# Kernel optimization log

Hardware: AMD Instinct MI355X
Metric: run time of the kernel (lower is better)

## Reference

```python
import jax, jax.numpy as jnp
import numpy as np

N_NODES = 100000
N_EDGES = 3200000
D_IN = 64
D_Z = 64
D_OUT = 3
SQRT_D = 0.1
SIGMA = (0.01, 0.01, 0.01)


def _seg_softmax(scores, seg, n):
    # softmax over edges grouped by destination node (PyG `softmax`)
    m = jax.ops.segment_max(scores, seg, num_segments=n)
    e = jnp.exp(scores - m[seg])
    s = jax.ops.segment_sum(e, seg, num_segments=n)
    return e / (s[seg] + 1e-16)


def _tconv(x, src, dst, Wq, bq, Wk, bk, Wv, bv, Ws, bs):
    # PyG TransformerConv, heads=1, concat=True, root_weight=True, beta=False
    n = x.shape[0]
    c = Wq.shape[1]
    q = x @ Wq + bq                                   # [N, C]
    k = x @ Wk + bk
    v = x @ Wv + bv
    scores = jnp.sum(q[dst] * k[src], axis=-1) / jnp.sqrt(jnp.asarray(c, x.dtype))  # [E]
    alpha = _seg_softmax(scores, dst, n)              # [E]
    agg = jax.ops.segment_sum(v[src] * alpha[:, None], dst, num_segments=n)  # [N, C]
    return agg + x @ Ws + bs                          # skip connection (lin_skip)


def _lin_params(key, din, dout):
    kw, kb = jax.random.split(key)
    scale = 1.0 / np.sqrt(din)
    W = jax.random.uniform(kw, (din, dout), jnp.float32, -scale, scale)
    b = jax.random.uniform(kb, (dout,), jnp.float32, -scale, scale)
    return W, b


def setup_inputs() -> dict:
    key = jax.random.key(0)
    keys = jax.random.split(key, 16)
    x = jax.random.normal(keys[0], (N_NODES, D_IN), jnp.float32)
    edge_index = jax.random.randint(keys[1], (2, N_EDGES), 0, N_NODES, jnp.int32)
    noise = jax.random.normal(keys[2], (N_NODES, D_OUT), jnp.float32)
    inp = {"x": x, "edge_index": edge_index, "noise": noise}
    dims = [(D_IN, D_Z), (D_Z, D_Z), (D_Z, D_OUT)]
    ki = 3
    for li, (din, dout) in enumerate(dims, start=1):
        for nm in ("q", "k", "v", "s"):
            W, b = _lin_params(keys[ki], din, dout)
            ki += 1
            inp[f"W{li}{nm}"] = W
            inp[f"b{li}{nm}"] = b
    return inp


def reference(x, edge_index, noise,
              W1q, b1q, W1k, b1k, W1v, b1v, W1s, b1s,
              W2q, b2q, W2k, b2k, W2v, b2v, W2s, b2s,
              W3q, b3q, W3k, b3k, W3v, b3v, W3s, b3s):
    src, dst = edge_index[0], edge_index[1]
    h = jnp.tanh(_tconv(x, src, dst, W1q, b1q, W1k, b1k, W1v, b1v, W1s, b1s))
    h = jnp.tanh(_tconv(h, src, dst, W2q, b2q, W2k, b2k, W2v, b2v, W2s, b2s) + h)
    drift = _tconv(h, src, dst, W3q, b3q, W3k, b3k, W3v, b3v, W3s, b3s)  # [N, 3]
    sigma = jnp.asarray(SIGMA, drift.dtype)
    z = noise * sigma  # per-column noise scaling (std_z > 1e-4 branch)
    return drift + z / SQRT_D
```

## Files before the change

kernel.cpp:

```cpp
#include <hip/hip_runtime.h>

#define N_NODES 100000
#define N_EDGES 3200000
#define NBUK 391
#define NPB 256
#define CHUNK 8192
#define NCHUNK 391

#if defined(__has_builtin)
#if __has_builtin(__builtin_amdgcn_fdot2_f32_bf16)
#define HAS_DOT2 1
#endif
#endif
#ifndef HAS_DOT2
#define HAS_DOT2 0
#endif

__device__ __forceinline__ float bf2f(unsigned short u) {
  return __uint_as_float(((unsigned)u) << 16);
}
__device__ __forceinline__ unsigned short f2bf(float f) {
  unsigned u = __float_as_uint(f);
  u += 0x7fffu + ((u >> 16) & 1u);
  return (unsigned short)(u >> 16);
}
__device__ __forceinline__ float lo16(unsigned u) { return __uint_as_float(u << 16); }
__device__ __forceinline__ float hi16(unsigned u) { return __uint_as_float(u & 0xffff0000u); }


__global__ void k_detect(const unsigned short* __restrict__ xu, int* __restrict__ flag) {
  __shared__ int cnt;
  if (threadIdx.x == 0) cnt = 0;
  __syncthreads();
  int c = 0;
  for (int i = threadIdx.x; i < 4096; i += 256) {
    float v = fabsf(bf2f(xu[2 * i]));
    if (v >= 1e-4f && v <= 10.f) c++;
  }
  atomicAdd(&cnt, c);
  __syncthreads();
  if (threadIdx.x == 0) *flag = (cnt > 2048) ? 1 : 0;
}


__global__ __launch_bounds__(512) void k_cvt_x(const void* __restrict__ x,
                                               unsigned short* __restrict__ xb,
                                               const int* __restrict__ flag) {
  int i = blockIdx.x * 512 + threadIdx.x;
  if (i >= N_NODES * 8) return;
  if (*flag) {
    ((uint4*)xb)[i] = ((const uint4*)x)[i];
  } else {
    const float4* xf = (const float4*)x;
    float4 a = xf[2 * i], b = xf[2 * i + 1];
    uint4 o;
    o.x = (unsigned)f2bf(a.x) | ((unsigned)f2bf(a.y) << 16);
    o.y = (unsigned)f2bf(a.z) | ((unsigned)f2bf(a.w) << 16);
    o.z = (unsigned)f2bf(b.x) | ((unsigned)f2bf(b.y) << 16);
    o.w = (unsigned)f2bf(b.z) | ((unsigned)f2bf(b.w) << 16);
    ((uint4*)xb)[i] = o;
  }
}

struct CvtArgs {
  const void* src[24];
  int dstoff[24];
  int n[24];
  int pp[24];
};

__global__ void k_cvt_w(CvtArgs a, unsigned short* __restrict__ wb,
                        const int* __restrict__ flag) {
  int b = blockIdx.x;
  const void* s = a.src[b];
  int n = a.n[b];
  int pp = a.pp[b];
  unsigned short* d = wb + a.dstoff[b];
  int isbf = *flag;
  for (int i = threadIdx.x; i < n; i += 256) {
    unsigned short v = isbf ? ((const unsigned short*)s)[i] : f2bf(((const float*)s)[i]);
    if (pp) {
      int k = i >> 6, c = i & 63;
      d[((k >> 1) << 7) + (c << 1) + (k & 1)] = v;
    } else {
      d[i] = v;
    }
  }
}


__global__ __launch_bounds__(256) void k_bhist(const int* __restrict__ dsts,
                                               int* __restrict__ counts) {
  __shared__ int hist[NBUK];
  for (int i = threadIdx.x; i < NBUK; i += 256) hist[i] = 0;
  __syncthreads();
  int e0 = blockIdx.x * CHUNK;
  int n = min(CHUNK, N_EDGES - e0);
  for (int i = threadIdx.x; i < n; i += 256)
    atomicAdd(&hist[dsts[e0 + i] >> 8], 1);
  __syncthreads();
  for (int i = threadIdx.x; i < NBUK; i += 256)
    counts[blockIdx.x * NBUK + i] = hist[i];
}

__global__ __launch_bounds__(64) void k_bscanA(int* __restrict__ counts,
                                               int* __restrict__ tot) {
  int b = blockIdx.x;
  int lane = threadIdx.x;
  int carry = 0;
  for (int c0 = 0; c0 < NCHUNK; c0 += 64) {
    int c = c0 + lane;
    int v = (c < NCHUNK) ? counts[c * NBUK + b] : 0;
    int s = v;
#pragma unroll
    for (int o = 1; o < 64; o <<= 1) {
      int u = __shfl_up(s, o, 64);
      if (lane >= o) s += u;
    }
    if (c < NCHUNK) counts[c * NBUK + b] = s - v + carry;
    carry += __shfl(s, 63, 64);
  }
  if (lane == 0) tot[b] = carry;
}

__global__ void k_bscanB(const int* __restrict__ tot, int* __restrict__ bbase) {
  __shared__ int s[512];
  int t = threadIdx.x;
  int v = (t < NBUK) ? tot[t] : 0;
  s[t] = v;
  __syncthreads();
  for (int o = 1; o < 512; o <<= 1) {
    int u = (t >= o) ? s[t - o] : 0;
    __syncthreads();
    s[t] += u;
    __syncthreads();
  }
  if (t <= NBUK) bbase[t] = s[t] - v;
}

__global__ __launch_bounds__(256) void k_bscat(const int* __restrict__ srcs,
                                               const int* __restrict__ dsts,
                                               const int* __restrict__ counts,
                                               const int* __restrict__ bbase,
                                               unsigned* __restrict__ blist) {
  __shared__ int cnt[NBUK];
  for (int i = threadIdx.x; i < NBUK; i += 256)
    cnt[i] = counts[blockIdx.x * NBUK + i] + bbase[i];
  __syncthreads();
  int e0 = blockIdx.x * CHUNK;
  int n = min(CHUNK, N_EDGES - e0);
  for (int i = threadIdx.x; i < n; i += 256) {
    int s = srcs[e0 + i];
    int d = dsts[e0 + i];
    int p = atomicAdd(&cnt[d >> 8], 1);
    blist[p] = ((unsigned)s << 8) | (unsigned)(d & 255);
  }
}

__global__ __launch_bounds__(256) void k_bfinal(const unsigned* __restrict__ blist,
                                                const int* __restrict__ bbase,
                                                int* __restrict__ off,
                                                int* __restrict__ csr) {
  __shared__ int hcnt[NPB];
  __shared__ int sc[NPB];
  int t = threadIdx.x;
  int b = blockIdx.x;
  int s = bbase[b], e = bbase[b + 1];
  hcnt[t] = 0;
  __syncthreads();
  for (int i = s + t; i < e; i += 256)
    atomicAdd(&hcnt[blist[i] & 255], 1);
  __syncthreads();
  int v = hcnt[t];
  sc[t] = v;
  __syncthreads();
  for (int o = 1; o < 256; o <<= 1) {
    int u = (t >= o) ? sc[t - o] : 0;
    __syncthreads();
    sc[t] += u;
    __syncthreads();
  }
  int my = s + sc[t] - v;
  int node = b * NPB + t;
  if (node < N_NODES) off[node] = my;
  if (b == 0 && t == 0) off[N_NODES] = bbase[NBUK];
  sc[t] = my;
  __syncthreads();
  for (int i = s + t; i < e; i += 256) {
    unsigned u = blist[i];
    int p = atomicAdd(&sc[u & 255], 1);
    csr[p] = (int)(u >> 8);
  }
}


#if HAS_DOT2
typedef __bf16 bf16x2 __attribute__((ext_vector_type(2)));
__device__ __forceinline__ float dot2bf(unsigned h2, unsigned w2, float acc) {
  return __builtin_amdgcn_fdot2_f32_bf16(__builtin_bit_cast(bf16x2, h2),
                                         __builtin_bit_cast(bf16x2, w2), acc, false);
}
#else
__device__ __forceinline__ float dot2bf(unsigned h2, unsigned w2, float acc) {
  acc += lo16(h2) * lo16(w2);
  acc += hi16(h2) * hi16(w2);
  return acc;
}
#endif

__global__ __launch_bounds__(256) void k_gemmkvqs(
    const unsigned short* __restrict__ hin,
    const unsigned* __restrict__ PQ2, const unsigned* __restrict__ PK2,
    const unsigned* __restrict__ PV2, const unsigned* __restrict__ PS2,
    const unsigned short* __restrict__ bq, const unsigned short* __restrict__ bk,
    const unsigned short* __restrict__ bv, const unsigned short* __restrict__ bs,
    unsigned short* __restrict__ Kt, unsigned short* __restrict__ Vt,
    float* __restrict__ Qt, float* __restrict__ St) {
  int wid = blockIdx.x * 4 + (threadIdx.x >> 6);
  int lane = threadIdx.x & 63;
  int r0 = wid * 4;
  const unsigned* hrow = (const unsigned*)(hin + (size_t)r0 * 64);
  unsigned hp0 = hrow[lane & 31];
  unsigned hp1 = hrow[32 + (lane & 31)];
  unsigned hp2 = hrow[64 + (lane & 31)];
  unsigned hp3 = hrow[96 + (lane & 31)];
  float bqv = bf2f(bq[lane]), bkv = bf2f(bk[lane]);
  float bvv = bf2f(bv[lane]), bsv = bf2f(bs[lane]);
  float qa0 = bqv, qa1 = bqv, qa2 = bqv, qa3 = bqv;
  float ka0 = bkv, ka1 = bkv, ka2 = bkv, ka3 = bkv;
  float va0 = bvv, va1 = bvv, va2 = bvv, va3 = bvv;
  float sa0 = bsv, sa1 = bsv, sa2 = bsv, sa3 = bsv;
  for (int kk = 0; kk < 32; ++kk) {
    unsigned wq = PQ2[kk * 64 + lane];
    unsigned wk = PK2[kk * 64 + lane];
    unsigned wv = PV2[kk * 64 + lane];
    unsigned ws = PS2[kk * 64 + lane];
    unsigned hb0 = __shfl(hp0, kk, 64);
    unsigned hb1 = __shfl(hp1, kk, 64);
    unsigned hb2 = __shfl(hp2, kk, 64);
    unsigned hb3 = __shfl(hp3, kk, 64);
    qa0 = dot2bf(hb0, wq, qa0); ka0 = dot2bf(hb0, wk, ka0);
    va0 = dot2bf(hb0, wv, va0); sa0 = dot2bf(hb0, ws, sa0);
    qa1 = dot2bf(hb1, wq, qa1); ka1 = dot2bf(hb1, wk, ka1);
    va1 = dot2bf(hb1, wv, va1); sa1 = dot2bf(hb1, ws, sa1);
    qa2 = dot2bf(hb2, wq, qa2); ka2 = dot2bf(hb2, wk, ka2);
    va2 = dot2bf(hb2, wv, va2); sa2 = dot2bf(hb2, ws, sa2);
    qa3 = dot2bf(hb3, wq, qa3); ka3 = dot2bf(hb3, wk, ka3);
    va3 = dot2bf(hb3, wv, va3); sa3 = dot2bf(hb3, ws, sa3);
  }
  Kt[(size_t)(r0 + 0) * 64 + lane] = f2bf(ka0);
  Kt[(size_t)(r0 + 1) * 64 + lane] = f2bf(ka1);
  Kt[(size_t)(r0 + 2) * 64 + lane] = f2bf(ka2);
  Kt[(size_t)(r0 + 3) * 64 + lane] = f2bf(ka3);
  Vt[(size_t)(r0 + 0) * 64 + lane] = f2bf(va0);
  Vt[(size_t)(r0 + 1) * 64 + lane] = f2bf(va1);
  Vt[(size_t)(r0 + 2) * 64 + lane] = f2bf(va2);
  Vt[(size_t)(r0 + 3) * 64 + lane] = f2bf(va3);
  Qt[(size_t)(r0 + 0) * 64 + lane] = qa0;
  Qt[(size_t)(r0 + 1) * 64 + lane] = qa1;
  Qt[(size_t)(r0 + 2) * 64 + lane] = qa2;
  Qt[(size_t)(r0 + 3) * 64 + lane] = qa3;
  St[(size_t)(r0 + 0) * 64 + lane] = sa0;
  St[(size_t)(r0 + 1) * 64 + lane] = sa1;
  St[(size_t)(r0 + 2) * 64 + lane] = sa2;
  St[(size_t)(r0 + 3) * 64 + lane] = sa3;
}


template <bool RES>
__global__ __launch_bounds__(256) void k_edge64b(
    const int* __restrict__ off, const int* __restrict__ csr,
    const unsigned short* __restrict__ hin,
    const float* __restrict__ Qt, const float* __restrict__ St,
    const unsigned short* __restrict__ Kt, const unsigned short* __restrict__ Vt,
    unsigned short* __restrict__ hout) {
  __shared__ float qs[4][64];
  int w = threadIdx.x >> 6;
  int lane = threadIdx.x & 63;
  int wid = blockIdx.x * 4 + w;
  int base = off[wid];
  int deg = off[wid + 1] - base;
  int nsrc = csr[base + ((lane < deg) ? lane : 0)];
  float q = Qt[(size_t)wid * 64 + lane];
  float sk = St[(size_t)wid * 64 + lane];
  float hv = 0.f;
  if (RES) hv = bf2f(hin[(size_t)wid * 64 + lane]);
  qs[w][lane] = q;

  float m = -1e30f, ssum = 0.f;
  float4 acc = {0.f, 0.f, 0.f, 0.f};
  int g = lane >> 4;
  int c16 = lane & 15;
  int g8 = lane >> 3;
  int c8 = lane & 7;
  const float4* qv = (const float4*)qs[w];
  float4 qA = qv[2 * c8];
  float4 qB = qv[2 * c8 + 1];

  for (int j0 = 0; j0 < deg; j0 += 64) {
    int cnt = min(64, deg - j0);
    int src = nsrc;
    int nj = j0 + 64;
    if (nj < deg)
      nsrc = csr[base + nj + ((lane < deg - nj) ? lane : 0)];
    float sc = 0.f;
    int nit = (cnt + 7) >> 3;
    for (int t = 0; t < nit; ++t) {
      int st = __shfl(src, 8 * t + g8, 64);
      uint4 kk = *(const uint4*)(Kt + (size_t)st * 64 + c8 * 8);
      float p = qA.x * lo16(kk.x) + qA.y * hi16(kk.x)
              + qA.z * lo16(kk.y) + qA.w * hi16(kk.y)
              + qB.x * lo16(kk.z) + qB.y * hi16(kk.z)
              + qB.z * lo16(kk.w) + qB.w * hi16(kk.w);
      p += __shfl_xor(p, 4, 64);
      p += __shfl_xor(p, 2, 64);
      p += __shfl_xor(p, 1, 64);
      float got = __shfl(p, (lane & 7) << 3, 64);
      if ((lane >> 3) == t) sc = got;
    }
    sc *= 0.125f;
    sc = fminf(fmaxf(sc, -60.f), 60.f);
    if (lane >= cnt) sc = -1e30f;
    float bm = sc;
    bm = fmaxf(bm, __shfl_xor(bm, 32, 64));
    bm = fmaxf(bm, __shfl_xor(bm, 16, 64));
    bm = fmaxf(bm, __shfl_xor(bm, 8, 64));
    bm = fmaxf(bm, __shfl_xor(bm, 4, 64));
    bm = fmaxf(bm, __shfl_xor(bm, 2, 64));
    bm = fmaxf(bm, __shfl_xor(bm, 1, 64));
    float mn = fmaxf(m, bm);
    float al = __expf(sc - mn);
    float bsum = al;
    bsum += __shfl_xor(bsum, 32, 64);
    bsum += __shfl_xor(bsum, 16, 64);
    bsum += __shfl_xor(bsum, 8, 64);
    bsum += __shfl_xor(bsum, 4, 64);
    bsum += __shfl_xor(bsum, 2, 64);
    bsum += __shfl_xor(bsum, 1, 64);
    float corr = __expf(m - mn);
    ssum = ssum * corr + bsum;
    acc.x *= corr;
    acc.y *= corr;
    acc.z *= corr;
    acc.w *= corr;
    m = mn;
    for (int jj = 0; jj < cnt; jj += 16) {
      int e0 = jj + g, e1 = jj + 4 + g, e2 = jj + 8 + g, e3 = jj + 12 + g;
      int s0 = __shfl(src, e0, 64);
      int s1 = __shfl(src, e1, 64);
      int s2 = __shfl(src, e2, 64);
      int s3 = __shfl(src, e3, 64);
      float a0 = __shfl(al, e0, 64);
      float a1 = __shfl(al, e1, 64);
      float a2 = __shfl(al, e2, 64);
      float a3 = __shfl(al, e3, 64);
      uint2 v0 = *(const uint2*)(Vt + (size_t)s0 * 64 + c16 * 4);
      uint2 v1 = *(const uint2*)(Vt + (size_t)s1 * 64 + c16 * 4);
      uint2 v2 = *(const uint2*)(Vt + (size_t)s2 * 64 + c16 * 4);
      uint2 v3 = *(const uint2*)(Vt + (size_t)s3 * 64 + c16 * 4);
      acc.x += a0 * lo16(v0.x); acc.y += a0 * hi16(v0.x);
      acc.z += a0 * lo16(v0.y); acc.w += a0 * hi16(v0.y);
      acc.x += a1 * lo16(v1.x); acc.y += a1 * hi16(v1.x);
      acc.z += a1 * lo16(v1.y); acc.w += a1 * hi16(v1.y);
      acc.x += a2 * lo16(v2.x); acc.y += a2 * hi16(v2.x);
      acc.z += a2 * lo16(v2.y); acc.w += a2 * hi16(v2.y);
      acc.x += a3 * lo16(v3.x); acc.y += a3 * hi16(v3.x);
      acc.z += a3 * lo16(v3.y); acc.w += a3 * hi16(v3.y);
    }
  }
  acc.x += __shfl_xor(acc.x, 16, 64);
  acc.y += __shfl_xor(acc.y, 16, 64);
  acc.z += __shfl_xor(acc.z, 16, 64);
  acc.w += __shfl_xor(acc.w, 16, 64);
  acc.x += __shfl_xor(acc.x, 32, 64);
  acc.y += __shfl_xor(acc.y, 32, 64);
  acc.z += __shfl_xor(acc.z, 32, 64);
  acc.w += __shfl_xor(acc.w, 32, 64);
  float f0 = __shfl(acc.x, lane >> 2, 64);
  float f1 = __shfl(acc.y, lane >> 2, 64);
  float f2 = __shfl(acc.z, lane >> 2, 64);
  float f3 = __shfl(acc.w, lane >> 2, 64);
  int cc = lane & 3;
  float aggv = (cc == 0) ? f0 : ((cc == 1) ? f1 : ((cc == 2) ? f2 : f3));
  float val = aggv / (ssum + 1e-16f) + sk;
  if (RES) val += hv;
  hout[(size_t)wid * 64 + lane] = f2bf(tanhf(val));
}


__global__ __launch_bounds__(256) void k_gemm3(
    const unsigned short* __restrict__ hin,
    const unsigned short* __restrict__ Wq, const unsigned short* __restrict__ bq,
    const unsigned short* __restrict__ Wk, const unsigned short* __restrict__ bk,
    const unsigned short* __restrict__ Wv, const unsigned short* __restrict__ bv,
    const unsigned short* __restrict__ Ws, const unsigned short* __restrict__ bs,
    float* __restrict__ Q3, float* __restrict__ S3, uint4* __restrict__ KV3) {
  int r = blockIdx.x * 4 + (threadIdx.x >> 6);
  int lane = threadIdx.x & 63;
  float hj = bf2f(hin[(size_t)r * 64 + lane]);
  float p[12];
#pragma unroll
  for (int c = 0; c < 3; ++c) {
    p[c]     = hj * bf2f(Wq[lane * 3 + c]);
    p[3 + c] = hj * bf2f(Wk[lane * 3 + c]);
    p[6 + c] = hj * bf2f(Wv[lane * 3 + c]);
    p[9 + c] = hj * bf2f(Ws[lane * 3 + c]);
  }
#pragma unroll
  for (int o = 32; o >= 1; o >>= 1) {
#pragma unroll
    for (int i = 0; i < 12; ++i) p[i] += __shfl_xor(p[i], o, 64);
  }
  if (lane == 0) {
    float kk[3], vv[3];
    for (int c = 0; c < 3; ++c) {
      Q3[r * 4 + c] = p[c] + bf2f(bq[c]);
      S3[r * 4 + c] = p[9 + c] + bf2f(bs[c]);
      kk[c] = p[3 + c] + bf2f(bk[c]);
      vv[c] = p[6 + c] + bf2f(bv[c]);
    }
    uint4 pk;
    pk.x = (unsigned)f2bf(kk[0]) | ((unsigned)f2bf(vv[0]) << 16);
    pk.y = (unsigned)f2bf(kk[1]) | ((unsigned)f2bf(vv[1]) << 16);
    pk.z = (unsigned)f2bf(kk[2]) | ((unsigned)f2bf(vv[2]) << 16);
    pk.w = 0;
    KV3[r] = pk;
  }
}


__global__ __launch_bounds__(256) void k_edge3(
    const int* __restrict__ off, const int* __restrict__ csr,
    const float* __restrict__ Q3, const float* __restrict__ S3,
    const uint4* __restrict__ KV3, const void* __restrict__ noise,
    void* __restrict__ out, const int* __restrict__ flag) {
  int w = threadIdx.x >> 6;
  int lane = threadIdx.x & 63;
  int d = blockIdx.x * 4 + w;
  int base = off[d];
  int deg = off[d + 1] - base;
  float q0 = Q3[d * 4], q1 = Q3[d * 4 + 1], q2 = Q3[d * 4 + 2];
  const float isq = 0.57735026919f;
  float m = -1e30f, ssum = 0.f, a0 = 0.f, a1 = 0.f, a2 = 0.f;
  for (int j0 = 0; j0 < deg; j0 += 64) {
    int cnt = min(64, deg - j0);
    int src = csr[base + ((lane < cnt) ? (j0 + lane) : 0)];
    uint4 kv = KV3[src];
    float sc = (q0 * lo16(kv.x) + q1 * lo16(kv.y) + q2 * lo16(kv.z)) * isq;
    sc = fminf(fmaxf(sc, -60.f), 60.f);
    if (lane >= cnt) sc = -1e30f;
    float bm = sc;
#pragma unroll
    for (int o = 32; o >= 1; o >>= 1) bm = fmaxf(bm, __shfl_xor(bm, o, 64));
    float mn = fmaxf(m, bm);
    float al = __expf(sc - mn);
    float p0 = al * hi16(kv.x);
    float p1 = al * hi16(kv.y);
    float p2 = al * hi16(kv.z);
    float bsum = al;
#pragma unroll
    for (int o = 32; o >= 1; o >>= 1) {
      bsum += __shfl_xor(bsum, o, 64);
      p0 += __shfl_xor(p0, o, 64);
      p1 += __shfl_xor(p1, o, 64);
      p2 += __shfl_xor(p2, o, 64);
    }
    float corr = __expf(m - mn);
    ssum = ssum * corr + bsum;
    a0 = a0 * corr + p0;
    a1 = a1 * corr + p1;
    a2 = a2 * corr + p2;
    m = mn;
  }
  if (lane == 0) {
    float inv = 1.f / (ssum + 1e-16f);
    int isbf = *flag;
    float n0, n1, n2;
    if (isbf) {
      const unsigned short* nu = (const unsigned short*)noise;
      n0 = bf2f(nu[d * 3 + 0]);
      n1 = bf2f(nu[d * 3 + 1]);
      n2 = bf2f(nu[d * 3 + 2]);
    } else {
      const float* nf = (const float*)noise;
      n0 = nf[d * 3 + 0];
      n1 = nf[d * 3 + 1];
      n2 = nf[d * 3 + 2];
    }
    float r0 = a0 * inv + S3[d * 4 + 0] + 0.1f * n0;
    float r1 = a1 * inv + S3[d * 4 + 1] + 0.1f * n1;
    float r2 = a2 * inv + S3[d * 4 + 2] + 0.1f * n2;
    if (isbf) {
      unsigned short* ou = (unsigned short*)out;
      ou[d * 3 + 0] = f2bf(r0);
      ou[d * 3 + 1] = f2bf(r1);
      ou[d * 3 + 2] = f2bf(r2);
    } else {
      float* of = (float*)out;
      of[d * 3 + 0] = r0;
      of[d * 3 + 1] = r1;
      of[d * 3 + 2] = r2;
    }
  }
}


extern "C" void kernel_launch(void* const* d_in, const int* in_sizes, int n_in,
                              void* d_out, int out_size, void* d_ws, size_t ws_size,
                              hipStream_t stream) {
  const int* ei = (const int*)d_in[1];
  const int* srcs = ei;
  const int* dsts = ei + N_EDGES;

  char* w = (char*)d_ws;
  int* off = (int*)w;
  int* csr = (int*)(w + 400128);
  char* hreg = w + 13200128;
  unsigned short* h = (unsigned short*)hreg;
  int* counts = (int*)(hreg + 524288);
  int* bbase = (int*)(hreg + 1200128);
  int* tot = (int*)(hreg + 1310720);
  char* kvbase = w + 26000128;
  unsigned* blist = (unsigned*)kvbase;
  unsigned short* Kt = (unsigned short*)kvbase;
  unsigned short* Vt = (unsigned short*)(kvbase + 12800000);
  float* Q3 = (float*)kvbase;
  float* S3 = (float*)(kvbase + 2097152);
  uint4* KV3 = (uint4*)(kvbase + 4194304);
  unsigned short* wb = (unsigned short*)(w + 51600128);
  int* flag = (int*)(w + 51668352);
  float* Qt = (float*)(w + 51668480);
  float* St = (float*)(w + 77268480);
  const size_t NEED_BIG = 102868480;
  if (ws_size < NEED_BIG) return;

  CvtArgs ca;
  {
    int idx = 0;
    for (int l = 0; l < 2; ++l) {
      int base = l * 16640;
      for (int p = 0; p < 4; ++p) {
        ca.src[idx] = d_in[3 + l * 8 + p * 2];
        ca.dstoff[idx] = base + p * 4096;
        ca.n[idx] = 4096;
        ca.pp[idx] = 1;
        idx++;
        ca.src[idx] = d_in[3 + l * 8 + p * 2 + 1];
        ca.dstoff[idx] = base + 16384 + p * 64;
        ca.n[idx] = 64;
        ca.pp[idx] = 0;
        idx++;
      }
    }
    int o = 33280;
    for (int p = 0; p < 4; ++p) {
      ca.src[idx] = d_in[3 + 16 + p * 2];
      ca.dstoff[idx] = o;
      ca.n[idx] = 192;
      ca.pp[idx] = 0;
      o += 192;
      idx++;
      ca.src[idx] = d_in[3 + 16 + p * 2 + 1];
      ca.dstoff[idx] = o;
      ca.n[idx] = 3;
      ca.pp[idx] = 0;
      o += 3;
      idx++;
    }
  }
  const unsigned* PQ20 = (const unsigned*)(wb);
  const unsigned* PK20 = (const unsigned*)(wb + 4096);
  const unsigned* PV20 = (const unsigned*)(wb + 8192);
  const unsigned* PS20 = (const unsigned*)(wb + 12288);
  const unsigned* PQ21 = (const unsigned*)(wb + 16640);
  const unsigned* PK21 = (const unsigned*)(wb + 16640 + 4096);
  const unsigned* PV21 = (const unsigned*)(wb + 16640 + 8192);
  const unsigned* PS21 = (const unsigned*)(wb + 16640 + 12288);
  const unsigned short* Bq0 = wb + 16384;
  const unsigned short* Bk0 = wb + 16448;
  const unsigned short* Bv0 = wb + 16512;
  const unsigned short* Bs0 = wb + 16576;
  const unsigned short* Bq1 = wb + 16640 + 16384;
  const unsigned short* Bk1 = wb + 16640 + 16448;
  const unsigned short* Bv1 = wb + 16640 + 16512;
  const unsigned short* Bs1 = wb + 16640 + 16576;
  const unsigned short* W3q = wb + 33280;
  const unsigned short* B3q = wb + 33472;
  const unsigned short* W3k = wb + 33475;
  const unsigned short* B3k = wb + 33667;
  const unsigned short* W3v = wb + 33670;
  const unsigned short* B3v = wb + 33862;
  const unsigned short* W3s = wb + 33865;
  const unsigned short* B3s = wb + 34057;

  k_detect<<<1, 256, 0, stream>>>((const unsigned short*)d_in[0], flag);
  k_cvt_w<<<24, 256, 0, stream>>>(ca, wb, flag);

  k_bhist<<<NCHUNK, 256, 0, stream>>>(dsts, counts);
  k_bscanA<<<NBUK, 64, 0, stream>>>(counts, tot);
  k_bscanB<<<1, 512, 0, stream>>>(tot, bbase);
  k_bscat<<<NCHUNK, 256, 0, stream>>>(srcs, dsts, counts, bbase, blist);
  k_bfinal<<<NBUK, 256, 0, stream>>>(blist, bbase, off, csr);

  k_cvt_x<<<(N_NODES * 8 + 511) / 512, 512, 0, stream>>>(d_in[0], h, flag);

  const int gw = N_NODES / 4;
  const int gp = N_NODES / 16;
  k_gemmkvqs<<<gp, 256, 0, stream>>>(h, PQ20, PK20, PV20, PS20,
                                     Bq0, Bk0, Bv0, Bs0, Kt, Vt, Qt, St);
  k_edge64b<false><<<gw, 256, 0, stream>>>(off, csr, h, Qt, St, Kt, Vt, h);
  k_gemmkvqs<<<gp, 256, 0, stream>>>(h, PQ21, PK21, PV21, PS21,
                                     Bq1, Bk1, Bv1, Bs1, Kt, Vt, Qt, St);
  k_edge64b<true><<<gw, 256, 0, stream>>>(off, csr, h, Qt, St, Kt, Vt, h);
  k_gemm3<<<gw, 256, 0, stream>>>(h, W3q, B3q, W3k, B3k, W3v, B3v, W3s, B3s,
                                  Q3, S3, KV3);
  k_edge3<<<gw, 256, 0, stream>>>(off, csr, Q3, S3, KV3, d_in[2], d_out, flag);
}
```

Measured before the change: 649.4 us.

## Fuse x conversion into first GEMM, widen GEMM rows, repack layer-3 weights

Removes the separate x-to-bf16 conversion kernel by converting fp32 input rows inside the first projection GEMM. The GEMM now handles 8 rows per wave instead of 4, so each weight load serves more rows. The layer-3 projection is rewritten to pack its weights as bf16 pairs and spread each node's dot products over 4 lanes with dot2, replacing the full 64-lane reductions. The edge kernel also broadcasts q with shuffles instead of staging it through shared memory. The costs are more register pressure in the GEMM and extra shuffles in the edge kernel.

```diff
diff --git a/kernel.cpp b/kernel.cpp
--- a/kernel.cpp
+++ b/kernel.cpp
@@ -40,26 +40,6 @@
   atomicAdd(&cnt, c);
   __syncthreads();
   if (threadIdx.x == 0) *flag = (cnt > 2048) ? 1 : 0;
-}
-
-
-__global__ __launch_bounds__(512) void k_cvt_x(const void* __restrict__ x,
-                                               unsigned short* __restrict__ xb,
-                                               const int* __restrict__ flag) {
-  int i = blockIdx.x * 512 + threadIdx.x;
-  if (i >= N_NODES * 8) return;
-  if (*flag) {
-    ((uint4*)xb)[i] = ((const uint4*)x)[i];
-  } else {
-    const float4* xf = (const float4*)x;
-    float4 a = xf[2 * i], b = xf[2 * i + 1];
-    uint4 o;
-    o.x = (unsigned)f2bf(a.x) | ((unsigned)f2bf(a.y) << 16);
-    o.y = (unsigned)f2bf(a.z) | ((unsigned)f2bf(a.w) << 16);
-    o.z = (unsigned)f2bf(b.x) | ((unsigned)f2bf(b.y) << 16);
-    o.w = (unsigned)f2bf(b.z) | ((unsigned)f2bf(b.w) << 16);
-    ((uint4*)xb)[i] = o;
-  }
 }
 
 struct CvtArgs {
@@ -79,9 +59,12 @@
   int isbf = *flag;
   for (int i = threadIdx.x; i < n; i += 256) {
     unsigned short v = isbf ? ((const unsigned short*)s)[i] : f2bf(((const float*)s)[i]);
-    if (pp) {
+    if (pp == 1) {
       int k = i >> 6, c = i & 63;
       d[((k >> 1) << 7) + (c << 1) + (k & 1)] = v;
+    } else if (pp >= 3) {
+      int dd = i / 3, c = i % 3 + (pp - 3);
+      d[(dd >> 1) * 24 + (c << 1) + (dd & 1)] = v;
     } else {
       d[i] = v;
     }
@@ -208,8 +191,9 @@
 }
 #endif
 
+template <bool L1>
 __global__ __launch_bounds__(256) void k_gemmkvqs(
-    const unsigned short* __restrict__ hin,
+    const void* __restrict__ xin, const int* __restrict__ flag,
     const unsigned* __restrict__ PQ2, const unsigned* __restrict__ PK2,
     const unsigned* __restrict__ PV2, const unsigned* __restrict__ PS2,
     const unsigned short* __restrict__ bq, const unsigned short* __restrict__ bk,
@@ -218,52 +202,54 @@
     float* __restrict__ Qt, float* __restrict__ St) {
   int wid = blockIdx.x * 4 + (threadIdx.x >> 6);
   int lane = threadIdx.x & 63;
-  int r0 = wid * 4;
-  const unsigned* hrow = (const unsigned*)(hin + (size_t)r0 * 64);
-  unsigned hp0 = hrow[lane & 31];
-  unsigned hp1 = hrow[32 + (lane & 31)];
-  unsigned hp2 = hrow[64 + (lane & 31)];
-  unsigned hp3 = hrow[96 + (lane & 31)];
+  int r0 = wid * 8;
+  int l31 = lane & 31;
+  unsigned hp[8];
+  bool cvt = L1 && (*flag == 0);
+  if (cvt) {
+    const float2* xf = (const float2*)xin;
+#pragma unroll
+    for (int j = 0; j < 8; ++j) {
+      float2 v = xf[(size_t)(r0 + j) * 32 + l31];
+      hp[j] = (unsigned)f2bf(v.x) | ((unsigned)f2bf(v.y) << 16);
+    }
+  } else {
+    const unsigned* hu = (const unsigned*)xin;
+#pragma unroll
+    for (int j = 0; j < 8; ++j)
+      hp[j] = hu[(size_t)(r0 + j) * 32 + l31];
+  }
   float bqv = bf2f(bq[lane]), bkv = bf2f(bk[lane]);
   float bvv = bf2f(bv[lane]), bsv = bf2f(bs[lane]);
-  float qa0 = bqv, qa1 = bqv, qa2 = bqv, qa3 = bqv;
-  float ka0 = bkv, ka1 = bkv, ka2 = bkv, ka3 = bkv;
-  float va0 = bvv, va1 = bvv, va2 = bvv, va3 = bvv;
-  float sa0 = bsv, sa1 = bsv, sa2 = bsv, sa3 = bsv;
+  float qa[8], ka[8], va[8], sa[8];
+#pragma unroll
+  for (int j = 0; j < 8; ++j) {
+    qa[j] = bqv;
+    ka[j] = bkv;
+    va[j] = bvv;
+    sa[j] = bsv;
+  }
   for (int kk = 0; kk < 32; ++kk) {
     unsigned wq = PQ2[kk * 64 + lane];
     unsigned wk = PK2[kk * 64 + lane];
     unsigned wv = PV2[kk * 64 + lane];
     unsigned ws = PS2[kk * 64 + lane];
-    unsigned hb0 = __shfl(hp0, kk, 64);
-    unsigned hb1 = __shfl(hp1, kk, 64);
-    unsigned hb2 = __shfl(hp2, kk, 64);
-    unsigned hb3 = __shfl(hp3, kk, 64);
-    qa0 = dot2bf(hb0, wq, qa0); ka0 = dot2bf(hb0, wk, ka0);
-    va0 = dot2bf(hb0, wv, va0); sa0 = dot2bf(hb0, ws, sa0);
-    qa1 = dot2bf(hb1, wq, qa1); ka1 = dot2bf(hb1, wk, ka1);
-    va1 = dot2bf(hb1, wv, va1); sa1 = dot2bf(hb1, ws, sa1);
-    qa2 = dot2bf(hb2, wq, qa2); ka2 = dot2bf(hb2, wk, ka2);
-    va2 = dot2bf(hb2, wv, va2); sa2 = dot2bf(hb2, ws, sa2);
-    qa3 = dot2bf(hb3, wq, qa3); ka3 = dot2bf(hb3, wk, ka3);
-    va3 = dot2bf(hb3, wv, va3); sa3 = dot2bf(hb3, ws, sa3);
-  }
-  Kt[(size_t)(r0 + 0) * 64 + lane] = f2bf(ka0);
-  Kt[(size_t)(r0 + 1) * 64 + lane] = f2bf(ka1);
-  Kt[(size_t)(r0 + 2) * 64 + lane] = f2bf(ka2);
-  Kt[(size_t)(r0 + 3) * 64 + lane] = f2bf(ka3);
-  Vt[(size_t)(r0 + 0) * 64 + lane] = f2bf(va0);
-  Vt[(size_t)(r0 + 1) * 64 + lane] = f2bf(va1);
-  Vt[(size_t)(r0 + 2) * 64 + lane] = f2bf(va2);
-  Vt[(size_t)(r0 + 3) * 64 + lane] = f2bf(va3);
-  Qt[(size_t)(r0 + 0) * 64 + lane] = qa0;
-  Qt[(size_t)(r0 + 1) * 64 + lane] = qa1;
-  Qt[(size_t)(r0 + 2) * 64 + lane] = qa2;
-  Qt[(size_t)(r0 + 3) * 64 + lane] = qa3;
-  St[(size_t)(r0 + 0) * 64 + lane] = sa0;
-  St[(size_t)(r0 + 1) * 64 + lane] = sa1;
-  St[(size_t)(r0 + 2) * 64 + lane] = sa2;
-  St[(size_t)(r0 + 3) * 64 + lane] = sa3;
+#pragma unroll
+    for (int j = 0; j < 8; ++j) {
+      unsigned hb = __shfl(hp[j], kk, 64);
+      qa[j] = dot2bf(hb, wq, qa[j]);
+      ka[j] = dot2bf(hb, wk, ka[j]);
+      va[j] = dot2bf(hb, wv, va[j]);
+      sa[j] = dot2bf(hb, ws, sa[j]);
+    }
+  }
+#pragma unroll
+  for (int j = 0; j < 8; ++j) {
+    Kt[(size_t)(r0 + j) * 64 + lane] = f2bf(ka[j]);
+    Vt[(size_t)(r0 + j) * 64 + lane] = f2bf(va[j]);
+    Qt[(size_t)(r0 + j) * 64 + lane] = qa[j];
+    St[(size_t)(r0 + j) * 64 + lane] = sa[j];
+  }
 }
 
 
@@ -274,7 +260,6 @@
     const float* __restrict__ Qt, const float* __restrict__ St,
     const unsigned short* __restrict__ Kt, const unsigned short* __restrict__ Vt,
     unsigned short* __restrict__ hout) {
-  __shared__ float qs[4][64];
   int w = threadIdx.x >> 6;
   int lane = threadIdx.x & 63;
   int wid = blockIdx.x * 4 + w;
@@ -285,7 +270,6 @@
   float sk = St[(size_t)wid * 64 + lane];
   float hv = 0.f;
   if (RES) hv = bf2f(hin[(size_t)wid * 64 + lane]);
-  qs[w][lane] = q;
 
   float m = -1e30f, ssum = 0.f;
   float4 acc = {0.f, 0.f, 0.f, 0.f};
@@ -293,9 +277,16 @@
   int c16 = lane & 15;
   int g8 = lane >> 3;
   int c8 = lane & 7;
-  const float4* qv = (const float4*)qs[w];
-  float4 qA = qv[2 * c8];
-  float4 qB = qv[2 * c8 + 1];
+  int b8 = c8 << 3;
+  float4 qA, qB;
+  qA.x = __shfl(q, b8 + 0, 64);
+  qA.y = __shfl(q, b8 + 1, 64);
+  qA.z = __shfl(q, b8 + 2, 64);
+  qA.w = __shfl(q, b8 + 3, 64);
+  qB.x = __shfl(q, b8 + 4, 64);
+  qB.y = __shfl(q, b8 + 5, 64);
+  qB.z = __shfl(q, b8 + 6, 64);
+  qB.w = __shfl(q, b8 + 7, 64);
 
   for (int j0 = 0; j0 < deg; j0 += 64) {
     int cnt = min(64, deg - j0);
@@ -389,42 +380,52 @@
 
 
 __global__ __launch_bounds__(256) void k_gemm3(
-    const unsigned short* __restrict__ hin,
-    const unsigned short* __restrict__ Wq, const unsigned short* __restrict__ bq,
-    const unsigned short* __restrict__ Wk, const unsigned short* __restrict__ bk,
-    const unsigned short* __restrict__ Wv, const unsigned short* __restrict__ bv,
-    const unsigned short* __restrict__ Ws, const unsigned short* __restrict__ bs,
+    const unsigned short* __restrict__ hin, const unsigned* __restrict__ W12p,
+    const unsigned short* __restrict__ bq, const unsigned short* __restrict__ bk,
+    const unsigned short* __restrict__ bv, const unsigned short* __restrict__ bs,
     float* __restrict__ Q3, float* __restrict__ S3, uint4* __restrict__ KV3) {
-  int r = blockIdx.x * 4 + (threadIdx.x >> 6);
+  int w = threadIdx.x >> 6;
   int lane = threadIdx.x & 63;
-  float hj = bf2f(hin[(size_t)r * 64 + lane]);
-  float p[12];
-#pragma unroll
-  for (int c = 0; c < 3; ++c) {
-    p[c]     = hj * bf2f(Wq[lane * 3 + c]);
-    p[3 + c] = hj * bf2f(Wk[lane * 3 + c]);
-    p[6 + c] = hj * bf2f(Wv[lane * 3 + c]);
-    p[9 + c] = hj * bf2f(Ws[lane * 3 + c]);
-  }
-#pragma unroll
-  for (int o = 32; o >= 1; o >>= 1) {
-#pragma unroll
-    for (int i = 0; i < 12; ++i) p[i] += __shfl_xor(p[i], o, 64);
-  }
-  if (lane == 0) {
+  int g = lane >> 2, q4 = lane & 3;
+  int node = blockIdx.x * 64 + w * 16 + g;
+  if (node >= N_NODES) return;
+  const uint4* hp = (const uint4*)(hin + (size_t)node * 64 + q4 * 16);
+  uint4 h0 = hp[0], h1 = hp[1];
+  unsigned hu[8] = {h0.x, h0.y, h0.z, h0.w, h1.x, h1.y, h1.z, h1.w};
+  float a[12];
+#pragma unroll
+  for (int c = 0; c < 12; ++c) a[c] = 0.f;
+#pragma unroll
+  for (int j = 0; j < 8; ++j) {
+    int pr = q4 * 8 + j;
+    const uint4* wp = (const uint4*)(W12p + pr * 12);
+    uint4 wa = wp[0], wbv = wp[1], wc = wp[2];
+    unsigned wu[12] = {wa.x, wa.y, wa.z, wa.w, wbv.x, wbv.y,
+                       wbv.z, wbv.w, wc.x, wc.y, wc.z, wc.w};
+#pragma unroll
+    for (int c = 0; c < 12; ++c) a[c] = dot2bf(hu[j], wu[c], a[c]);
+  }
+#pragma unroll
+  for (int c = 0; c < 12; ++c) {
+    a[c] += __shfl_xor(a[c], 1, 64);
+    a[c] += __shfl_xor(a[c], 2, 64);
+  }
+  if (q4 == 0) {
+    for (int c = 0; c < 3; ++c) Q3[node * 4 + c] = a[c] + bf2f(bq[c]);
+  } else if (q4 == 1) {
+    for (int c = 0; c < 3; ++c) S3[node * 4 + c] = a[9 + c] + bf2f(bs[c]);
+  } else if (q4 == 2) {
     float kk[3], vv[3];
     for (int c = 0; c < 3; ++c) {
-      Q3[r * 4 + c] = p[c] + bf2f(bq[c]);
-      S3[r * 4 + c] = p[9 + c] + bf2f(bs[c]);
-      kk[c] = p[3 + c] + bf2f(bk[c]);
-      vv[c] = p[6 + c] + bf2f(bv[c]);
+      kk[c] = a[3 + c] + bf2f(bk[c]);
+      vv[c] = a[6 + c] + bf2f(bv[c]);
     }
     uint4 pk;
     pk.x = (unsigned)f2bf(kk[0]) | ((unsigned)f2bf(vv[0]) << 16);
     pk.y = (unsigned)f2bf(kk[1]) | ((unsigned)f2bf(vv[1]) << 16);
     pk.z = (unsigned)f2bf(kk[2]) | ((unsigned)f2bf(vv[2]) << 16);
     pk.w = 0;
-    KV3[r] = pk;
+    KV3[node] = pk;
   }
 }
 
@@ -552,19 +553,16 @@
         idx++;
       }
     }
-    int o = 33280;
     for (int p = 0; p < 4; ++p) {
       ca.src[idx] = d_in[3 + 16 + p * 2];
-      ca.dstoff[idx] = o;
+      ca.dstoff[idx] = 33280;
       ca.n[idx] = 192;
-      ca.pp[idx] = 0;
-      o += 192;
+      ca.pp[idx] = 3 + p * 3;
       idx++;
       ca.src[idx] = d_in[3 + 16 + p * 2 + 1];
-      ca.dstoff[idx] = o;
+      ca.dstoff[idx] = 34048 + p * 3;
       ca.n[idx] = 3;
       ca.pp[idx] = 0;
-      o += 3;
       idx++;
     }
   }
@@ -584,13 +582,10 @@
   const unsigned short* Bk1 = wb + 16640 + 16448;
   const unsigned short* Bv1 = wb + 16640 + 16512;
   const unsigned short* Bs1 = wb + 16640 + 16576;
-  const unsigned short* W3q = wb + 33280;
-  const unsigned short* B3q = wb + 33472;
-  const unsigned short* W3k = wb + 33475;
-  const unsigned short* B3k = wb + 33667;
-  const unsigned short* W3v = wb + 33670;
-  const unsigned short* B3v = wb + 33862;
-  const unsigned short* W3s = wb + 33865;
+  const unsigned* W12p = (const unsigned*)(wb + 33280);
+  const unsigned short* B3q = wb + 34048;
+  const unsigned short* B3k = wb + 34051;
+  const unsigned short* B3v = wb + 34054;
   const unsigned short* B3s = wb + 34057;
 
   k_detect<<<1, 256, 0, stream>>>((const unsigned short*)d_in[0], flag);
@@ -602,17 +597,15 @@
   k_bscat<<<NCHUNK, 256, 0, stream>>>(srcs, dsts, counts, bbase, blist);
   k_bfinal<<<NBUK, 256, 0, stream>>>(blist, bbase, off, csr);
 
-  k_cvt_x<<<(N_NODES * 8 + 511) / 512, 512, 0, stream>>>(d_in[0], h, flag);
-
   const int gw = N_NODES / 4;
-  const int gp = N_NODES / 16;
-  k_gemmkvqs<<<gp, 256, 0, stream>>>(h, PQ20, PK20, PV20, PS20,
-                                     Bq0, Bk0, Bv0, Bs0, Kt, Vt, Qt, St);
+  const int gp = N_NODES / 32;
+  const int g3 = (N_NODES + 63) / 64;
+  k_gemmkvqs<true><<<gp, 256, 0, stream>>>(d_in[0], flag, PQ20, PK20, PV20, PS20,
+                                           Bq0, Bk0, Bv0, Bs0, Kt, Vt, Qt, St);
   k_edge64b<false><<<gw, 256, 0, stream>>>(off, csr, h, Qt, St, Kt, Vt, h);
-  k_gemmkvqs<<<gp, 256, 0, stream>>>(h, PQ21, PK21, PV21, PS21,
-                                     Bq1, Bk1, Bv1, Bs1, Kt, Vt, Qt, St);
+  k_gemmkvqs<false><<<gp, 256, 0, stream>>>(h, flag, PQ21, PK21, PV21, PS21,
+                                            Bq1, Bk1, Bv1, Bs1, Kt, Vt, Qt, St);
   k_edge64b<true><<<gw, 256, 0, stream>>>(off, csr, h, Qt, St, Kt, Vt, h);
-  k_gemm3<<<gw, 256, 0, stream>>>(h, W3q, B3q, W3k, B3k, W3v, B3v, W3s, B3s,
-                                  Q3, S3, KV3);
+  k_gemm3<<<g3, 256, 0, stream>>>(h, W12p, B3q, B3k, B3v, B3s, Q3, S3, KV3);
   k_edge3<<<gw, 256, 0, stream>>>(off, csr, Q3, S3, KV3, d_in[2], d_out, flag);
 }
```

After: 592.2 us. -8.8%, faster.
